# Kernel tuning notes

Hardware: AMD Instinct MI355X
Metric: run time of the kernel (lower is better)

## Reference

```python
import jax, jax.numpy as jnp
import numpy as np

B, L, C, H, W = 2, 2048, 768, 8, 8
D_INNER, D_STATE, D_CONV, DT_RANK = 2 * C, 16, 4, (C + 15) // 16  # mamba defaults: expand=2, d_state=16, d_conv=4, dt_rank=ceil(C/16)


def setup_inputs() -> dict:
    key = jax.random.key(0)
    ks = jax.random.split(key, 9)
    s = 0.02
    x = jax.random.normal(ks[0], (B, L, C, H, W), dtype=jnp.float32)
    W_in = jax.random.normal(ks[1], (2 * D_INNER, C), dtype=jnp.float32) * s
    conv_w = jax.random.normal(ks[2], (D_INNER, D_CONV), dtype=jnp.float32) * s
    conv_b = jnp.zeros((D_INNER,), dtype=jnp.float32)
    W_xproj = jax.random.normal(ks[3], (DT_RANK + 2 * D_STATE, D_INNER), dtype=jnp.float32) * s
    W_dt = jax.random.normal(ks[4], (D_INNER, DT_RANK), dtype=jnp.float32) * s
    b_dt = jax.random.uniform(ks[5], (D_INNER,), dtype=jnp.float32, minval=-4.0, maxval=-2.0)
    A_log = jnp.log(jnp.broadcast_to(jnp.arange(1, D_STATE + 1, dtype=jnp.float32), (D_INNER, D_STATE)))
    D_param = jnp.ones((D_INNER,), dtype=jnp.float32)
    W_out = jax.random.normal(ks[6], (C, D_INNER), dtype=jnp.float32) * s
    return {"x": x, "W_in": W_in, "conv_w": conv_w, "conv_b": conv_b,
            "W_xproj": W_xproj, "W_dt": W_dt, "b_dt": b_dt,
            "A_log": A_log, "D_param": D_param, "W_out": W_out}


def _mamba(xc, W_in, conv_w, conv_b, W_xproj, W_dt, b_dt, A_log, D_param, W_out):
    # xc: [B, L, C]
    xz = jnp.einsum('blc,dc->bld', xc, W_in)              # [B,L,2*d_inner]
    xh, z = xz[..., :D_INNER], xz[..., D_INNER:]
    # causal depthwise conv1d over L, kernel size D_CONV
    xp = jnp.pad(xh, ((0, 0), (D_CONV - 1, 0), (0, 0)))
    xconv = conv_b
    for k in range(D_CONV):  # tiny fixed kernel loop
        xconv = xconv + xp[:, k:k + L, :] * conv_w[:, k]
    xh = jax.nn.silu(xconv)                                # [B,L,d_inner]
    xdb = jnp.einsum('bld,ed->ble', xh, W_xproj)
    dt = xdb[..., :DT_RANK]
    Bs = xdb[..., DT_RANK:DT_RANK + D_STATE]               # [B,L,d_state]
    Cs = xdb[..., DT_RANK + D_STATE:]                      # [B,L,d_state]
    delta = jax.nn.softplus(jnp.einsum('blr,dr->bld', dt, W_dt) + b_dt)  # [B,L,d_inner]
    A = -jnp.exp(A_log)                                    # [d_inner,d_state]

    def step(h, inp):
        d_t, B_t, C_t, x_t = inp                           # [B,d_inner],[B,s],[B,s],[B,d_inner]
        dA = jnp.exp(d_t[..., None] * A)                   # [B,d_inner,d_state]
        h = dA * h + (d_t * x_t)[..., None] * B_t[:, None, :]
        y = jnp.einsum('bds,bs->bd', h, C_t)
        return h, y

    h0 = jnp.zeros((xc.shape[0], D_INNER, D_STATE), dtype=xc.dtype)
    xs = (delta.transpose(1, 0, 2), Bs.transpose(1, 0, 2),
          Cs.transpose(1, 0, 2), xh.transpose(1, 0, 2))
    _, ys = jax.lax.scan(step, h0, xs)                     # ys: [L,B,d_inner]
    y = ys.transpose(1, 0, 2) + xh * D_param
    y = y * jax.nn.silu(z)
    return jnp.einsum('bld,cd->blc', y, W_out)             # [B,L,C]


def reference(x, W_in, conv_w, conv_b, W_xproj, W_dt, b_dt, A_log, D_param, W_out):
    # AdaptiveAvgPool2d((1,1)) + Flatten -> global mean over H,W
    xc = x.mean(axis=(-2, -1))                             # [B,L,C]
    return _mamba(xc, W_in, conv_w, conv_b, W_xproj, W_dt, b_dt, A_log, D_param, W_out)
```

## Files before the change

### kernel.cpp

```cpp
#include <hip/hip_runtime.h>
#include <cstddef>
#include <cstdint>

#define B_   2
#define L_   2048
#define C_   768
#define DI   1536
#define DS   16
#define DC   4
#define DTR  48
#define E2   3072
#define NXP  80
#define NCH  128
#define LCH  16
#define ML   (B_*L_)

typedef __bf16 bf16x8 __attribute__((ext_vector_type(8)));
typedef float  f32x4  __attribute__((ext_vector_type(4)));

__global__ __launch_bounds__(256) void k_reduce(const float4* __restrict__ x,
                                                float* __restrict__ xc) {
  int gid = blockIdx.x * 256 + threadIdx.x;
  float4 v = x[gid];
  float s = (v.x + v.y) + (v.z + v.w);
  s += __shfl_xor(s, 1, 16);
  s += __shfl_xor(s, 2, 16);
  s += __shfl_xor(s, 4, 16);
  s += __shfl_xor(s, 8, 16);
  if ((threadIdx.x & 15) == 0) xc[gid >> 4] = s * (1.0f / 64.0f);
}

static __device__ __forceinline__ ushort f2bf(float x) {
  uint32_t u = __builtin_bit_cast(uint32_t, x);
  u += 0x7fffu + ((u >> 16) & 1u);
  return (ushort)(u >> 16);
}

__global__ __launch_bounds__(256) void k_split(const float4* __restrict__ src,
                                               ushort4* __restrict__ hi,
                                               ushort4* __restrict__ lo) {
  int i = blockIdx.x * 256 + threadIdx.x;
  float4 v = src[i];
  ushort4 h, l;
  h.x = f2bf(v.x); l.x = f2bf(v.x - __builtin_bit_cast(float, (uint32_t)h.x << 16));
  h.y = f2bf(v.y); l.y = f2bf(v.y - __builtin_bit_cast(float, (uint32_t)h.y << 16));
  h.z = f2bf(v.z); l.z = f2bf(v.z - __builtin_bit_cast(float, (uint32_t)h.z << 16));
  h.w = f2bf(v.w); l.w = f2bf(v.w - __builtin_bit_cast(float, (uint32_t)h.w << 16));
  hi[i] = h; lo[i] = l;
}

static __device__ __forceinline__ void gl16(const ushort* g, ushort* l) {
  __builtin_amdgcn_global_load_lds(
      (const __attribute__((address_space(1))) uint32_t*)g,
      (__attribute__((address_space(3))) uint32_t*)l, 16, 0, 0);
}

__global__ __launch_bounds__(256) void k_gemm_mfma(
    const ushort* __restrict__ Ah, const ushort* __restrict__ Al,
    const ushort* __restrict__ Bh, const ushort* __restrict__ Bl,
    float* __restrict__ C, int N, int K) {
  __shared__ ushort lds[4 * 4096];
  const int tid  = threadIdx.x;
  const int lane = tid & 63;
  const int wid  = tid >> 6;
  const int wr = wid >> 1, wc = wid & 1;
  const int m0 = blockIdx.x * 128, n0 = blockIdx.y * 128;

  f32x4 acc[4][4];
#pragma unroll
  for (int i = 0; i < 4; ++i)
#pragma unroll
    for (int j = 0; j < 4; ++j) acc[i][j] = (f32x4){0.f, 0.f, 0.f, 0.f};

  const int srow  = tid & 127;
  const int shalf = tid >> 7;
  const size_t rowA = (size_t)(m0 + srow) * K;
  const size_t rowB = (size_t)(n0 + srow) * K;

  const int q = lane >> 4, r = lane & 15;
  const int fragA = q * 1024 + (wr * 64 + r) * 8;
  const int fragB = q * 1024 + (wc * 64 + r) * 8;

  for (int k0 = 0; k0 < K; k0 += 32) {
    __syncthreads();
#pragma unroll
    for (int t = 0; t < 2; ++t) {
      const int ko = k0 + (t * 2 + shalf) * 8;
      gl16(Ah + rowA + ko, &lds[0 * 4096 + t * 2048 + tid * 8]);
      gl16(Al + rowA + ko, &lds[1 * 4096 + t * 2048 + tid * 8]);
      gl16(Bh + rowB + ko, &lds[2 * 4096 + t * 2048 + tid * 8]);
      gl16(Bl + rowB + ko, &lds[3 * 4096 + t * 2048 + tid * 8]);
    }
    __syncthreads();

    bf16x8 ah[4], al[4], bh[4], bl[4];
#pragma unroll
    for (int i = 0; i < 4; ++i) {
      ah[i] = *(const bf16x8*)&lds[0 * 4096 + fragA + i * 128];
      al[i] = *(const bf16x8*)&lds[1 * 4096 + fragA + i * 128];
      bh[i] = *(const bf16x8*)&lds[2 * 4096 + fragB + i * 128];
      bl[i] = *(const bf16x8*)&lds[3 * 4096 + fragB + i * 128];
    }
#pragma unroll
    for (int i = 0; i < 4; ++i)
#pragma unroll
      for (int j = 0; j < 4; ++j)
        acc[i][j] = __builtin_amdgcn_mfma_f32_16x16x32_bf16(ah[i], bh[j], acc[i][j], 0, 0, 0);
#pragma unroll
    for (int i = 0; i < 4; ++i)
#pragma unroll
      for (int j = 0; j < 4; ++j)
        acc[i][j] = __builtin_amdgcn_mfma_f32_16x16x32_bf16(ah[i], bl[j], acc[i][j], 0, 0, 0);
#pragma unroll
    for (int i = 0; i < 4; ++i)
#pragma unroll
      for (int j = 0; j < 4; ++j)
        acc[i][j] = __builtin_amdgcn_mfma_f32_16x16x32_bf16(al[i], bh[j], acc[i][j], 0, 0, 0);
  }

  const int orow = m0 + wr * 64 + q * 4;
  const int ocol = n0 + wc * 64 + r;
#pragma unroll
  for (int i = 0; i < 4; ++i)
#pragma unroll
    for (int j = 0; j < 4; ++j) {
      float* cp = C + (size_t)(orow + i * 16) * N + (ocol + j * 16);
#pragma unroll
      for (int t = 0; t < 4; ++t) cp[(size_t)t * N] = acc[i][j][t];
    }
}

template <int BM, int BN, int TM, int TN, int MODE>
__global__ __launch_bounds__(256) void k_gemm(const float* __restrict__ A, int lda,
                                              const float* __restrict__ Bm, int ldb,
                                              float* __restrict__ Cm, int ldc,
                                              int M, int N, int K,
                                              const float* __restrict__ bias) {
  constexpr int BK = 16;
  __shared__ float As[BK][BM + 4];
  __shared__ float Bs[BK][BN + 4];
  const int tid = threadIdx.x;
  const int tx = tid & 15;
  const int ty = tid >> 4;
  const int m0 = blockIdx.x * BM;
  const int n0 = blockIdx.y * BN;

  float acc[TM][TN];
#pragma unroll
  for (int i = 0; i < TM; ++i)
#pragma unroll
    for (int j = 0; j < TN; ++j) acc[i][j] = 0.f;

  for (int k0 = 0; k0 < K; k0 += BK) {
#pragma unroll
    for (int t = 0; t < BM / 16; ++t) {
      int e = t * 256 + tid;
      int row = e >> 4, col = e & 15;
      int gm = m0 + row, gk = k0 + col;
      As[col][row] = (gm < M && gk < K) ? A[(size_t)gm * lda + gk] : 0.f;
    }
#pragma unroll
    for (int t = 0; t < BN / 16; ++t) {
      int e = t * 256 + tid;
      int row = e >> 4, col = e & 15;
      int gn = n0 + row, gk = k0 + col;
      Bs[col][row] = (gn < N && gk < K) ? Bm[(size_t)gn * ldb + gk] : 0.f;
    }
    __syncthreads();
#pragma unroll
    for (int kk = 0; kk < BK; ++kk) {
      float a[TM], bv[TN];
#pragma unroll
      for (int i = 0; i < TM; ++i) a[i] = As[kk][ty * TM + i];
#pragma unroll
      for (int j = 0; j < TN; ++j) bv[j] = Bs[kk][tx * TN + j];
#pragma unroll
      for (int i = 0; i < TM; ++i)
#pragma unroll
        for (int j = 0; j < TN; ++j) acc[i][j] = fmaf(a[i], bv[j], acc[i][j]);
    }
    __syncthreads();
  }
#pragma unroll
  for (int i = 0; i < TM; ++i) {
    int gm = m0 + ty * TM + i;
    if (gm >= M) continue;
#pragma unroll
    for (int j = 0; j < TN; ++j) {
      int gn = n0 + tx * TN + j;
      if (gn >= N) continue;
      float v = acc[i][j];
      if (MODE == 1) {
        v += bias[gn];
        v = fmaxf(v, 0.f) + log1pf(expf(-fabsf(v)));
      }
      Cm[(size_t)gm * ldc + gn] = v;
    }
  }
}

__global__ __launch_bounds__(256) void k_conv(const float* __restrict__ xz,
                                              const float* __restrict__ cw,
                                              const float* __restrict__ cb,
                                              float* __restrict__ xh) {
  int gid = blockIdx.x * 256 + threadIdx.x;
  int d = gid % DI;
  int bl = gid / DI;
  int l = bl % L_;
  const float* base = xz + (size_t)(bl - l) * E2 + d;
  float acc = cb[d];
#pragma unroll
  for (int k = 0; k < DC; ++k) {
    int ll = l + k - (DC - 1);
    float xv = (ll >= 0) ? base[(size_t)ll * E2] : 0.f;
    acc = fmaf(xv, cw[d * DC + k], acc);
  }
  float sig = 1.f / (1.f + expf(-acc));
  xh[gid] = acc * sig;
}

__global__ __launch_bounds__(256) void k_scan1(const float* __restrict__ delta,
                                               const float* __restrict__ xh,
                                               const float* __restrict__ xdb,
                                               const float* __restrict__ A_log,
                                               float* __restrict__ hend,
                                               float* __restrict__ sd) {
  int tid = threadIdx.x;
  int bid = blockIdx.x;
  int dblk = bid % (DI / 256);
  int c = (bid / (DI / 256)) % NCH;
  int b = bid / ((DI / 256) * NCH);
  int d = dblk * 256 + tid;

  float a[DS];
#pragma unroll
  for (int s = 0; s < DS; ++s) a[s] = -expf(A_log[d * DS + s]);
  float h[DS];
#pragma unroll
  for (int s = 0; s < DS; ++s) h[s] = 0.f;
  float sum_delta = 0.f;

  int l0 = c * LCH;
  for (int i = 0; i < LCH; ++i) {
    size_t bl = (size_t)b * L_ + (l0 + i);
    float dt = delta[bl * DI + d];
    float xv = xh[bl * DI + d];
    sum_delta += dt;
    float u = dt * xv;
    const float* Brow = xdb + bl * NXP + DTR;
#pragma unroll
    for (int s = 0; s < DS; ++s) {
      float dA = expf(dt * a[s]);
      h[s] = fmaf(dA, h[s], u * Brow[s]);
    }
  }
  size_t base = (size_t)(b * NCH + c) * DS * DI;
#pragma unroll
  for (int s = 0; s < DS; ++s) hend[base + (size_t)s * DI + d] = h[s];
  sd[(size_t)(b * NCH + c) * DI + d] = sum_delta;
}

__global__ __launch_bounds__(256) void k_scan2(const float* __restrict__ A_log,
                                               const float* __restrict__ sd,
                                               const float* __restrict__ hend,
                                               float* __restrict__ hinit) {
  int gid = blockIdx.x * 256 + threadIdx.x;
  int d = gid % DI;
  int s = (gid / DI) % DS;
  int b = gid / (DI * DS);
  float a = -expf(A_log[d * DS + s]);
  float h = 0.f;
  for (int c = 0; c < NCH; ++c) {
    size_t cb = (size_t)(b * NCH + c);
    size_t hidx = (cb * DS + s) * DI + d;
    hinit[hidx] = h;
    h = fmaf(expf(a * sd[cb * DI + d]), h, hend[hidx]);
  }
}

__global__ __launch_bounds__(256) void k_scan3(const float* __restrict__ delta,
                                               float* __restrict__ xh,
                                               const float* __restrict__ xdb,
                                               const float* __restrict__ xz,
                                               const float* __restrict__ A_log,
                                               const float* __restrict__ hinit,
                                               const float* __restrict__ Dp) {
  int tid = threadIdx.x;
  int bid = blockIdx.x;
  int dblk = bid % (DI / 256);
  int c = (bid / (DI / 256)) % NCH;
  int b = bid / ((DI / 256) * NCH);
  int d = dblk * 256 + tid;

  float a[DS];
#pragma unroll
  for (int s = 0; s < DS; ++s) a[s] = -expf(A_log[d * DS + s]);
  float h[DS];
  size_t hbase = (size_t)(b * NCH + c) * DS * DI;
#pragma unroll
  for (int s = 0; s < DS; ++s) h[s] = hinit[hbase + (size_t)s * DI + d];
  float dpar = Dp[d];

  int l0 = c * LCH;
  for (int i = 0; i < LCH; ++i) {
    size_t bl = (size_t)b * L_ + (l0 + i);
    float dt = delta[bl * DI + d];
    float xv = xh[bl * DI + d];
    float u = dt * xv;
    const float* row = xdb + bl * NXP;
    float y = 0.f;
#pragma unroll
    for (int s = 0; s < DS; ++s) {
      float dA = expf(dt * a[s]);
      h[s] = fmaf(dA, h[s], u * row[DTR + s]);
      y = fmaf(h[s], row[DTR + DS + s], y);
    }
    float z = xz[bl * E2 + DI + d];
    float sig = 1.f / (1.f + expf(-z));
    xh[bl * DI + d] = (y + xv * dpar) * (z * sig);
  }
}

extern "C" void kernel_launch(void* const* d_in, const int* in_sizes, int n_in,
                              void* d_out, int out_size, void* d_ws, size_t ws_size,
                              hipStream_t stream) {
  const float* x      = (const float*)d_in[0];
  const float* W_in   = (const float*)d_in[1];
  const float* conv_w = (const float*)d_in[2];
  const float* conv_b = (const float*)d_in[3];
  const float* W_xproj= (const float*)d_in[4];
  const float* W_dt   = (const float*)d_in[5];
  const float* b_dt   = (const float*)d_in[6];
  const float* A_log  = (const float*)d_in[7];
  const float* D_param= (const float*)d_in[8];
  const float* W_out  = (const float*)d_in[9];
  float* out = (float*)d_out;
  float* ws = (float*)d_ws;

  float* XC    = ws;
  float* XZ    = XC    + 3145728;
  float* XH    = XZ    + 12582912;
  float* XDB   = XH    + 6291456;
  float* DELTA = XDB   + 327680;
  float* SD    = DELTA + 6291456;
  float* HEND  = SD    + 393216;
  float* HINIT = HEND  + 6291456;

  ushort* XCh = (ushort*)HEND;
  ushort* XCl = XCh + 3145728;
  ushort* Wih = XCl + 3145728;
  ushort* Wil = Wih + 2359296;
  ushort* XHh = (ushort*)DELTA;
  ushort* XHl = XHh + 6291456;
  ushort* Woh = XHl + 6291456;
  ushort* Wol = Woh + 1179648;

  k_reduce<<<(B_*L_*C_*16)/256, 256, 0, stream>>>((const float4*)x, XC);
  k_split<<<3145728/1024, 256, 0, stream>>>((const float4*)XC,   (ushort4*)XCh, (ushort4*)XCl);
  k_split<<<2359296/1024, 256, 0, stream>>>((const float4*)W_in, (ushort4*)Wih, (ushort4*)Wil);
  k_gemm_mfma<<<dim3(ML/128, E2/128), 256, 0, stream>>>(XCh, XCl, Wih, Wil, XZ, E2, C_);
  k_conv<<<(B_*L_*DI)/256, 256, 0, stream>>>(XZ, conv_w, conv_b, XH);
  k_gemm<64,64,4,4,0><<<dim3(ML/64, 2), 256, 0, stream>>>(
      XH, DI, W_xproj, DI, XDB, NXP, ML, NXP, DI, nullptr);
  k_gemm<64,64,4,4,1><<<dim3(ML/64, DI/64), 256, 0, stream>>>(
      XDB, NXP, W_dt, DTR, DELTA, DI, ML, DI, DTR, b_dt);
  k_scan1<<<B_*NCH*(DI/256), 256, 0, stream>>>(DELTA, XH, XDB, A_log, HEND, SD);
  k_scan2<<<(B_*DS*DI)/256, 256, 0, stream>>>(A_log, SD, HEND, HINIT);
  k_scan3<<<B_*NCH*(DI/256), 256, 0, stream>>>(DELTA, XH, XDB, XZ, A_log, HINIT, D_param);
  k_split<<<6291456/1024, 256, 0, stream>>>((const float4*)XH,    (ushort4*)XHh, (ushort4*)XHl);
  k_split<<<1179648/1024, 256, 0, stream>>>((const float4*)W_out, (ushort4*)Woh, (ushort4*)Wol);
  k_gemm_mfma<<<dim3(ML/128, C_/128), 256, 0, stream>>>(XHh, XHl, Woh, Wol, out, C_, DI);
}
```

Before: 1.613 ms.

## Fuse bf16 splits into reduce and scan, double-buffer MFMA GEMM, grid-stride kernels

Several independent changes. The hi/lo bf16 split is now done inside the mean-reduction kernel and the final scan kernel, which removes two separate split passes and their fp32 round trips through memory. The MFMA GEMM gets double-buffered LDS so the next K-tile loads overlap compute, using twice the LDS per block. The reduce and conv kernels become grid-stride loops over a fixed grid, the x-projection GEMM tile drops to 32x64, and workspace aliasing is reshuffled to match.

Result: faster. 1.571 ms (-2.6%).

```diff
diff --git a/kernel.cpp b/kernel.cpp
--- a/kernel.cpp
+++ b/kernel.cpp
@@ -14,26 +14,40 @@
 #define NCH  128
 #define LCH  16
 #define ML   (B_*L_)
+#define GSB  2048
 
 typedef __bf16 bf16x8 __attribute__((ext_vector_type(8)));
 typedef float  f32x4  __attribute__((ext_vector_type(4)));
-
-__global__ __launch_bounds__(256) void k_reduce(const float4* __restrict__ x,
-                                                float* __restrict__ xc) {
-  int gid = blockIdx.x * 256 + threadIdx.x;
-  float4 v = x[gid];
-  float s = (v.x + v.y) + (v.z + v.w);
-  s += __shfl_xor(s, 1, 16);
-  s += __shfl_xor(s, 2, 16);
-  s += __shfl_xor(s, 4, 16);
-  s += __shfl_xor(s, 8, 16);
-  if ((threadIdx.x & 15) == 0) xc[gid >> 4] = s * (1.0f / 64.0f);
-}
 
 static __device__ __forceinline__ ushort f2bf(float x) {
   uint32_t u = __builtin_bit_cast(uint32_t, x);
   u += 0x7fffu + ((u >> 16) & 1u);
   return (ushort)(u >> 16);
+}
+static __device__ __forceinline__ float bf2f(ushort h) {
+  return __builtin_bit_cast(float, (uint32_t)h << 16);
+}
+
+__global__ __launch_bounds__(256) void k_reduce(const float4* __restrict__ x,
+                                                ushort* __restrict__ hi,
+                                                ushort* __restrict__ lo) {
+  constexpr int TOT = B_ * L_ * C_ * 16;
+  int tid = threadIdx.x;
+#pragma unroll 2
+  for (int gid = blockIdx.x * 256 + tid; gid < TOT; gid += GSB * 256) {
+    float4 v = x[gid];
+    float s = (v.x + v.y) + (v.z + v.w);
+    s += __shfl_xor(s, 1, 16);
+    s += __shfl_xor(s, 2, 16);
+    s += __shfl_xor(s, 4, 16);
+    s += __shfl_xor(s, 8, 16);
+    if ((tid & 15) == 0) {
+      float m = s * (1.0f / 64.0f);
+      ushort h = f2bf(m);
+      hi[gid >> 4] = h;
+      lo[gid >> 4] = f2bf(m - bf2f(h));
+    }
+  }
 }
 
 __global__ __launch_bounds__(256) void k_split(const float4* __restrict__ src,
@@ -42,10 +56,10 @@
   int i = blockIdx.x * 256 + threadIdx.x;
   float4 v = src[i];
   ushort4 h, l;
-  h.x = f2bf(v.x); l.x = f2bf(v.x - __builtin_bit_cast(float, (uint32_t)h.x << 16));
-  h.y = f2bf(v.y); l.y = f2bf(v.y - __builtin_bit_cast(float, (uint32_t)h.y << 16));
-  h.z = f2bf(v.z); l.z = f2bf(v.z - __builtin_bit_cast(float, (uint32_t)h.z << 16));
-  h.w = f2bf(v.w); l.w = f2bf(v.w - __builtin_bit_cast(float, (uint32_t)h.w << 16));
+  h.x = f2bf(v.x); l.x = f2bf(v.x - bf2f(h.x));
+  h.y = f2bf(v.y); l.y = f2bf(v.y - bf2f(h.y));
+  h.z = f2bf(v.z); l.z = f2bf(v.z - bf2f(h.z));
+  h.w = f2bf(v.w); l.w = f2bf(v.w - bf2f(h.w));
   hi[i] = h; lo[i] = l;
 }
 
@@ -59,7 +73,7 @@
     const ushort* __restrict__ Ah, const ushort* __restrict__ Al,
     const ushort* __restrict__ Bh, const ushort* __restrict__ Bl,
     float* __restrict__ C, int N, int K) {
-  __shared__ ushort lds[4 * 4096];
+  __shared__ ushort lds[2][4 * 4096];
   const int tid  = threadIdx.x;
   const int lane = tid & 63;
   const int wid  = tid >> 6;
@@ -81,25 +95,33 @@
   const int fragA = q * 1024 + (wr * 64 + r) * 8;
   const int fragB = q * 1024 + (wc * 64 + r) * 8;
 
-  for (int k0 = 0; k0 < K; k0 += 32) {
-    __syncthreads();
+  auto STAGE = [&](int buf, int k0) {
+    ushort* l = lds[buf];
 #pragma unroll
     for (int t = 0; t < 2; ++t) {
       const int ko = k0 + (t * 2 + shalf) * 8;
-      gl16(Ah + rowA + ko, &lds[0 * 4096 + t * 2048 + tid * 8]);
-      gl16(Al + rowA + ko, &lds[1 * 4096 + t * 2048 + tid * 8]);
-      gl16(Bh + rowB + ko, &lds[2 * 4096 + t * 2048 + tid * 8]);
-      gl16(Bl + rowB + ko, &lds[3 * 4096 + t * 2048 + tid * 8]);
-    }
+      gl16(Ah + rowA + ko, &l[0 * 4096 + t * 2048 + tid * 8]);
+      gl16(Al + rowA + ko, &l[1 * 4096 + t * 2048 + tid * 8]);
+      gl16(Bh + rowB + ko, &l[2 * 4096 + t * 2048 + tid * 8]);
+      gl16(Bl + rowB + ko, &l[3 * 4096 + t * 2048 + tid * 8]);
+    }
+  };
+
+  STAGE(0, 0);
+  const int nt = K >> 5;
+  int cur = 0;
+  for (int t = 0; t < nt; ++t) {
     __syncthreads();
-
+    if (t + 1 < nt) STAGE(cur ^ 1, (t + 1) * 32);
+
+    const ushort* l = lds[cur];
     bf16x8 ah[4], al[4], bh[4], bl[4];
 #pragma unroll
     for (int i = 0; i < 4; ++i) {
-      ah[i] = *(const bf16x8*)&lds[0 * 4096 + fragA + i * 128];
-      al[i] = *(const bf16x8*)&lds[1 * 4096 + fragA + i * 128];
-      bh[i] = *(const bf16x8*)&lds[2 * 4096 + fragB + i * 128];
-      bl[i] = *(const bf16x8*)&lds[3 * 4096 + fragB + i * 128];
+      ah[i] = *(const bf16x8*)&l[0 * 4096 + fragA + i * 128];
+      al[i] = *(const bf16x8*)&l[1 * 4096 + fragA + i * 128];
+      bh[i] = *(const bf16x8*)&l[2 * 4096 + fragB + i * 128];
+      bl[i] = *(const bf16x8*)&l[3 * 4096 + fragB + i * 128];
     }
 #pragma unroll
     for (int i = 0; i < 4; ++i)
@@ -116,6 +138,7 @@
 #pragma unroll
       for (int j = 0; j < 4; ++j)
         acc[i][j] = __builtin_amdgcn_mfma_f32_16x16x32_bf16(al[i], bh[j], acc[i][j], 0, 0, 0);
+    cur ^= 1;
   }
 
   const int orow = m0 + wr * 64 + q * 4;
@@ -203,20 +226,22 @@
                                               const float* __restrict__ cw,
                                               const float* __restrict__ cb,
                                               float* __restrict__ xh) {
-  int gid = blockIdx.x * 256 + threadIdx.x;
-  int d = gid % DI;
-  int bl = gid / DI;
-  int l = bl % L_;
-  const float* base = xz + (size_t)(bl - l) * E2 + d;
-  float acc = cb[d];
-#pragma unroll
-  for (int k = 0; k < DC; ++k) {
-    int ll = l + k - (DC - 1);
-    float xv = (ll >= 0) ? base[(size_t)ll * E2] : 0.f;
-    acc = fmaf(xv, cw[d * DC + k], acc);
-  }
-  float sig = 1.f / (1.f + expf(-acc));
-  xh[gid] = acc * sig;
+  constexpr int TOT = B_ * L_ * DI;
+  for (int gid = blockIdx.x * 256 + threadIdx.x; gid < TOT; gid += GSB * 256) {
+    int d = gid % DI;
+    int bl = gid / DI;
+    int l = bl % L_;
+    const float* base = xz + (size_t)(bl - l) * E2 + d;
+    float acc = cb[d];
+#pragma unroll
+    for (int k = 0; k < DC; ++k) {
+      int ll = l + k - (DC - 1);
+      float xv = (ll >= 0) ? base[(size_t)ll * E2] : 0.f;
+      acc = fmaf(xv, cw[d * DC + k], acc);
+    }
+    float sig = 1.f / (1.f + expf(-acc));
+    xh[gid] = acc * sig;
+  }
 }
 
 __global__ __launch_bounds__(256) void k_scan1(const float* __restrict__ delta,
@@ -279,12 +304,14 @@
 }
 
 __global__ __launch_bounds__(256) void k_scan3(const float* __restrict__ delta,
-                                               float* __restrict__ xh,
+                                               const float* __restrict__ xh,
                                                const float* __restrict__ xdb,
                                                const float* __restrict__ xz,
                                                const float* __restrict__ A_log,
                                                const float* __restrict__ hinit,
-                                               const float* __restrict__ Dp) {
+                                               const float* __restrict__ Dp,
+                                               ushort* __restrict__ yhi,
+                                               ushort* __restrict__ ylo) {
   int tid = threadIdx.x;
   int bid = blockIdx.x;
   int dblk = bid % (DI / 256);
@@ -317,7 +344,10 @@
     }
     float z = xz[bl * E2 + DI + d];
     float sig = 1.f / (1.f + expf(-z));
-    xh[bl * DI + d] = (y + xv * dpar) * (z * sig);
+    float yv = (y + xv * dpar) * (z * sig);
+    ushort hh = f2bf(yv);
+    yhi[bl * DI + d] = hh;
+    ylo[bl * DI + d] = f2bf(yv - bf2f(hh));
   }
 }
 
@@ -346,28 +376,27 @@
   float* HEND  = SD    + 393216;
   float* HINIT = HEND  + 6291456;
 
-  ushort* XCh = (ushort*)HEND;
+  ushort* XCh = (ushort*)XC;
   ushort* XCl = XCh + 3145728;
-  ushort* Wih = XCl + 3145728;
+  ushort* Wih = (ushort*)HEND;
   ushort* Wil = Wih + 2359296;
-  ushort* XHh = (ushort*)DELTA;
+  ushort* XHh = (ushort*)HEND;
   ushort* XHl = XHh + 6291456;
-  ushort* Woh = XHl + 6291456;
+  ushort* Woh = (ushort*)XC;
   ushort* Wol = Woh + 1179648;
 
-  k_reduce<<<(B_*L_*C_*16)/256, 256, 0, stream>>>((const float4*)x, XC);
-  k_split<<<3145728/1024, 256, 0, stream>>>((const float4*)XC,   (ushort4*)XCh, (ushort4*)XCl);
+  k_reduce<<<GSB, 256, 0, stream>>>((const float4*)x, XCh, XCl);
   k_split<<<2359296/1024, 256, 0, stream>>>((const float4*)W_in, (ushort4*)Wih, (ushort4*)Wil);
   k_gemm_mfma<<<dim3(ML/128, E2/128), 256, 0, stream>>>(XCh, XCl, Wih, Wil, XZ, E2, C_);
-  k_conv<<<(B_*L_*DI)/256, 256, 0, stream>>>(XZ, conv_w, conv_b, XH);
-  k_gemm<64,64,4,4,0><<<dim3(ML/64, 2), 256, 0, stream>>>(
+  k_conv<<<GSB, 256, 0, stream>>>(XZ, conv_w, conv_b, XH);
+  k_gemm<32,64,2,4,0><<<dim3(ML/32, 2), 256, 0, stream>>>(
       XH, DI, W_xproj, DI, XDB, NXP, ML, NXP, DI, nullptr);
   k_gemm<64,64,4,4,1><<<dim3(ML/64, DI/64), 256, 0, stream>>>(
       XDB, NXP, W_dt, DTR, DELTA, DI, ML, DI, DTR, b_dt);
   k_scan1<<<B_*NCH*(DI/256), 256, 0, stream>>>(DELTA, XH, XDB, A_log, HEND, SD);
   k_scan2<<<(B_*DS*DI)/256, 256, 0, stream>>>(A_log, SD, HEND, HINIT);
-  k_scan3<<<B_*NCH*(DI/256), 256, 0, stream>>>(DELTA, XH, XDB, XZ, A_log, HINIT, D_param);
-  k_split<<<6291456/1024, 256, 0, stream>>>((const float4*)XH,    (ushort4*)XHh, (ushort4*)XHl);
+  k_scan3<<<B_*NCH*(DI/256), 256, 0, stream>>>(DELTA, XH, XDB, XZ, A_log, HINIT,
+                                               D_param, XHh, XHl);
   k_split<<<1179648/1024, 256, 0, stream>>>((const float4*)W_out, (ushort4*)Woh, (ushort4*)Wol);
   k_gemm_mfma<<<dim3(ML/128, C_/128), 256, 0, stream>>>(XHh, XHl, Woh, Wol, out, C_, DI);
 }
```
